# Performance work log

Hardware: AMD Instinct MI355X
Metric: run time of the kernel (lower is better)

The kernel has to match this reference:

```python
import jax, jax.numpy as jnp
import numpy as np

LAMBD = 0.1  # lambd from __init__

N_POINTS = 262144
D_EMBED = 512
N_CLUSTERS = 64


def setup_inputs() -> dict:
    key = jax.random.key(0)
    k1, k2 = jax.random.split(key)
    x = jax.random.normal(k1, (N_POINTS, D_EMBED), dtype=jnp.float32)
    # original init: uniform(-1, 1)
    centroids = jax.random.uniform(k2, (N_CLUSTERS, D_EMBED), dtype=jnp.float32, minval=-1.0, maxval=1.0)
    return {"x": x, "centroids": centroids, "alpha": 100}


def reference(x, centroids, alpha):
    # stack_dist[i, n] = sum_d (x[n,d] - centroids[i,d])^2, fused via the
    x2 = jnp.sum(x * x, axis=1)                      # [N]
    c2 = jnp.sum(centroids * centroids, axis=1)      # [k]
    cross = jnp.einsum('nd,kd->kn', x, centroids)    # [k, N]
    dist = x2[None, :] + c2[:, None] - 2.0 * cross   # [k, N]
    # exp(-alpha*(dist - min)) / sum == softmax(-alpha*dist) along the k axis
    soft = jax.nn.softmax(-jnp.float32(alpha) * dist, axis=0)  # [k, N]
    k_means_loss = LAMBD * jnp.mean(jnp.sum(dist * soft, axis=0))
    return k_means_loss
```

## Files before the change

### kernel.cpp

```cpp
#include <hip/hip_runtime.h>
#include <hip/hip_bf16.h>

#define N_POINTS   262144
#define D_EMBED    512
#define N_CLUSTERS 64
#define LAMBD      0.1f

#define PTS_PER_WAVE  32
#define PTS_PER_BLK   128

typedef __attribute__((ext_vector_type(8)))  short short8;
typedef __attribute__((ext_vector_type(16))) float f32x16;

__device__ __forceinline__ unsigned short f2bf(float f) {
    union { float f; unsigned u; } v; v.f = f;
    unsigned u = v.u;
    return (unsigned short)((u + 0x7FFFu + ((u >> 16) & 1u)) >> 16);
}

__global__ void prep_kernel(const float* __restrict__ cent,
                            float* __restrict__ c2_ws,
                            unsigned short* __restrict__ afrag,
                            float* __restrict__ out) {
    const int k    = blockIdx.x;
    const int lane = threadIdx.x;
    const float* row = cent + (size_t)k * D_EMBED;

    float4 v0 = ((const float4*)row)[lane * 2 + 0];
    float4 v1 = ((const float4*)row)[lane * 2 + 1];

    float s = v0.x*v0.x + v0.y*v0.y + v0.z*v0.z + v0.w*v0.w
            + v1.x*v1.x + v1.y*v1.y + v1.z*v1.z + v1.w*v1.w;
    #pragma unroll
    for (int m = 1; m < 64; m <<= 1) s += __shfl_xor(s, m);
    if (lane == 0) c2_ws[k] = s;

    const int st = lane >> 1;
    const int h  = lane & 1;
    const int t  = k >> 5;
    const int m  = k & 31;
    const size_t idx8 = ((size_t)(st * 2 + t) * 64 + m + 32 * h) * 8;

    ushort4 h0, h1;
    h0.x = f2bf(v0.x); h0.y = f2bf(v0.y); h0.z = f2bf(v0.z); h0.w = f2bf(v0.w);
    h1.x = f2bf(v1.x); h1.y = f2bf(v1.y); h1.z = f2bf(v1.z); h1.w = f2bf(v1.w);
    *(ushort4*)&afrag[idx8 + 0] = h0;
    *(ushort4*)&afrag[idx8 + 4] = h1;

    if (k == 0 && lane == 0) *out = 0.0f;
}

__global__ __launch_bounds__(256, 4)
void main_kernel(const float* __restrict__ x,
                 const int* __restrict__ alpha_p,
                 const float* __restrict__ c2_ws,
                 const unsigned short* __restrict__ afrag,
                 float* __restrict__ out) {
    __shared__ float c2s[N_CLUSTERS];
    __shared__ float bsum[4];

    const int tid  = threadIdx.x;
    const int lane = tid & 63;
    const int w    = tid >> 6;

    if (tid < 64) c2s[tid] = c2_ws[tid];
    __syncthreads();

    const float alpha = (float)alpha_p[0];
    const int n = lane & 31;
    const int h = lane >> 5;
    const size_t pt = (size_t)blockIdx.x * PTS_PER_BLK + w * PTS_PER_WAVE + n;
    const float* xp = x + pt * D_EMBED + 8 * h;

    f32x16 acc0, acc1;
    #pragma unroll
    for (int r = 0; r < 16; ++r) { acc0[r] = 0.0f; acc1[r] = 0.0f; }

    float x2 = 0.0f;
    #pragma unroll 4
    for (int s = 0; s < 32; ++s) {
        float4 u0 = *(const float4*)(xp + 16 * s);
        float4 u1 = *(const float4*)(xp + 16 * s + 4);

        x2 += u0.x*u0.x + u0.y*u0.y + u0.z*u0.z + u0.w*u0.w
            + u1.x*u1.x + u1.y*u1.y + u1.z*u1.z + u1.w*u1.w;

        short8 b;
        b[0] = (short)f2bf(u0.x); b[1] = (short)f2bf(u0.y);
        b[2] = (short)f2bf(u0.z); b[3] = (short)f2bf(u0.w);
        b[4] = (short)f2bf(u1.x); b[5] = (short)f2bf(u1.y);
        b[6] = (short)f2bf(u1.z); b[7] = (short)f2bf(u1.w);

        short8 a0 = *(const short8*)&afrag[((size_t)(s * 2 + 0) * 64 + lane) * 8];
        short8 a1 = *(const short8*)&afrag[((size_t)(s * 2 + 1) * 64 + lane) * 8];

        acc0 = __builtin_amdgcn_mfma_f32_32x32x16_bf16(a0, b, acc0, 0, 0, 0);
        acc1 = __builtin_amdgcn_mfma_f32_32x32x16_bf16(a1, b, acc1, 0, 0, 0);
    }
    x2 += __shfl_xor(x2, 32);

    float minv = 1e30f;
    #pragma unroll
    for (int r = 0; r < 16; ++r) {
        const int rr = (r & 3) + 8 * (r >> 2) + 4 * h;
        const float d0 = x2 + c2s[rr]      - 2.0f * acc0[r];
        const float d1 = x2 + c2s[rr + 32] - 2.0f * acc1[r];
        acc0[r] = d0; acc1[r] = d1;
        minv = fminf(minv, fminf(d0, d1));
    }
    minv = fminf(minv, __shfl_xor(minv, 32));

    float esum = 0.0f, wsum = 0.0f;
    #pragma unroll
    for (int r = 0; r < 16; ++r) {
        const float e0 = __expf(-alpha * (acc0[r] - minv));
        const float e1 = __expf(-alpha * (acc1[r] - minv));
        esum += e0 + e1;
        wsum += acc0[r] * e0 + acc1[r] * e1;
    }
    esum += __shfl_xor(esum, 32);
    wsum += __shfl_xor(wsum, 32);

    float pv = wsum / esum;
    #pragma unroll
    for (int m = 1; m < 64; m <<= 1) pv += __shfl_xor(pv, m);

    if (lane == 0) bsum[w] = pv;
    __syncthreads();
    if (tid == 0) {
        const float T = bsum[0] + bsum[1] + bsum[2] + bsum[3];
        atomicAdd(out, T * (LAMBD / (2.0f * (float)N_POINTS)));
    }
}

extern "C" void kernel_launch(void* const* d_in, const int* in_sizes, int n_in,
                              void* d_out, int out_size, void* d_ws, size_t ws_size,
                              hipStream_t stream) {
    const float* x      = (const float*)d_in[0];
    const float* cent   = (const float*)d_in[1];
    const int*   alphap = (const int*)d_in[2];
    float* out = (float*)d_out;

    float*          c2_ws = (float*)d_ws;
    unsigned short* afrag = (unsigned short*)((char*)d_ws + 256);

    hipLaunchKernelGGL(prep_kernel, dim3(N_CLUSTERS), dim3(64), 0, stream,
                       cent, c2_ws, afrag, out);
    hipLaunchKernelGGL(main_kernel, dim3(N_POINTS / PTS_PER_BLK), dim3(256), 0, stream,
                       x, alphap, c2_ws, afrag, out);
}
```

Before: 691.8 us.

## Stage centroid fragments in LDS and double-buffer x loads in registers

Each block copies the full bf16 centroid fragment table (64 KB) into shared memory once, and the MFMA loop then reads A fragments from LDS instead of global memory. The x loads are software-pipelined: eight steps' worth of float4 pairs are prefetched into a register double buffer while the current group is computed. Launch bounds drop to 2 blocks per SM to allow the larger register footprint. The cost is 64 KB of LDS per block and fewer resident waves to hide memory latency, on a kernel that is bound by streaming 512 MB of x.

```diff
diff --git a/kernel.cpp b/kernel.cpp
--- a/kernel.cpp
+++ b/kernel.cpp
@@ -50,12 +50,13 @@
     if (k == 0 && lane == 0) *out = 0.0f;
 }
 
-__global__ __launch_bounds__(256, 4)
+__global__ __launch_bounds__(256, 2)
 void main_kernel(const float* __restrict__ x,
                  const int* __restrict__ alpha_p,
                  const float* __restrict__ c2_ws,
                  const unsigned short* __restrict__ afrag,
                  float* __restrict__ out) {
+    __shared__ unsigned short alds[64 * 64 * 8];
     __shared__ float c2s[N_CLUSTERS];
     __shared__ float bsum[4];
 
@@ -63,6 +64,11 @@
     const int lane = tid & 63;
     const int w    = tid >> 6;
 
+    #pragma unroll
+    for (int it = 0; it < 16; ++it) {
+        const int e8 = it * 256 + tid;
+        *(short8*)&alds[(size_t)e8 * 8] = *(const short8*)&afrag[(size_t)e8 * 8];
+    }
     if (tid < 64) c2s[tid] = c2_ws[tid];
     __syncthreads();
 
@@ -76,26 +82,46 @@
     #pragma unroll
     for (int r = 0; r < 16; ++r) { acc0[r] = 0.0f; acc1[r] = 0.0f; }
 
+    float4 buf[2][16];
+    #pragma unroll
+    for (int i = 0; i < 8; ++i) {
+        buf[0][2*i+0] = *(const float4*)(xp + 16 * i);
+        buf[0][2*i+1] = *(const float4*)(xp + 16 * i + 4);
+    }
+
     float x2 = 0.0f;
-    #pragma unroll 4
-    for (int s = 0; s < 32; ++s) {
-        float4 u0 = *(const float4*)(xp + 16 * s);
-        float4 u1 = *(const float4*)(xp + 16 * s + 4);
+    #pragma unroll
+    for (int g = 0; g < 4; ++g) {
+        const int cb = g & 1, nb = cb ^ 1;
+        if (g < 3) {
+            #pragma unroll
+            for (int i = 0; i < 8; ++i) {
+                const int s = (g + 1) * 8 + i;
+                buf[nb][2*i+0] = *(const float4*)(xp + 16 * s);
+                buf[nb][2*i+1] = *(const float4*)(xp + 16 * s + 4);
+            }
+        }
+        #pragma unroll
+        for (int i = 0; i < 8; ++i) {
+            const int s = g * 8 + i;
+            const float4 u0 = buf[cb][2*i+0];
+            const float4 u1 = buf[cb][2*i+1];
 
-        x2 += u0.x*u0.x + u0.y*u0.y + u0.z*u0.z + u0.w*u0.w
-            + u1.x*u1.x + u1.y*u1.y + u1.z*u1.z + u1.w*u1.w;
+            x2 += u0.x*u0.x + u0.y*u0.y + u0.z*u0.z + u0.w*u0.w
+                + u1.x*u1.x + u1.y*u1.y + u1.z*u1.z + u1.w*u1.w;
 
-        short8 b;
-        b[0] = (short)f2bf(u0.x); b[1] = (short)f2bf(u0.y);
-        b[2] = (short)f2bf(u0.z); b[3] = (short)f2bf(u0.w);
-        b[4] = (short)f2bf(u1.x); b[5] = (short)f2bf(u1.y);
-        b[6] = (short)f2bf(u1.z); b[7] = (short)f2bf(u1.w);
+            short8 b;
+            b[0] = (short)f2bf(u0.x); b[1] = (short)f2bf(u0.y);
+            b[2] = (short)f2bf(u0.z); b[3] = (short)f2bf(u0.w);
+            b[4] = (short)f2bf(u1.x); b[5] = (short)f2bf(u1.y);
+            b[6] = (short)f2bf(u1.z); b[7] = (short)f2bf(u1.w);
 
-        short8 a0 = *(const short8*)&afrag[((size_t)(s * 2 + 0) * 64 + lane) * 8];
-        short8 a1 = *(const short8*)&afrag[((size_t)(s * 2 + 1) * 64 + lane) * 8];
+            short8 a0 = *(const short8*)&alds[((size_t)(s * 2 + 0) * 64 + lane) * 8];
+            short8 a1 = *(const short8*)&alds[((size_t)(s * 2 + 1) * 64 + lane) * 8];
 
-        acc0 = __builtin_amdgcn_mfma_f32_32x32x16_bf16(a0, b, acc0, 0, 0, 0);
-        acc1 = __builtin_amdgcn_mfma_f32_32x32x16_bf16(a1, b, acc1, 0, 0, 0);
+            acc0 = __builtin_amdgcn_mfma_f32_32x32x16_bf16(a0, b, acc0, 0, 0, 0);
+            acc1 = __builtin_amdgcn_mfma_f32_32x32x16_bf16(a1, b, acc1, 0, 0, 0);
+        }
     }
     x2 += __shfl_xor(x2, 32);
 
```

New measurement: 679.3 us. About the same (-1.8%).
